# Optimization experiments

Hardware: AMD Instinct MI355X
Metric: run time of the kernel (lower is better)

Reference implementation:

```python
import jax, jax.numpy as jnp
import numpy as np

NEAR = 0.1
FAR = 100.0


def quat_to_rotmat(q):
    q = q / jnp.linalg.norm(q, axis=-1, keepdims=True)
    w, x, y, z = q[..., 0], q[..., 1], q[..., 2], q[..., 3]
    R = jnp.stack([
        1 - 2 * (y * y + z * z), 2 * (x * y - z * w), 2 * (x * z + y * w),
        2 * (x * y + z * w), 1 - 2 * (x * x + z * z), 2 * (y * z - x * w),
        2 * (x * z - y * w), 2 * (y * z + x * w), 1 - 2 * (x * x + y * y)
    ], axis=-1)
    return R.reshape(q.shape[:-1] + (3, 3))


def _render_view(means, scales, rots, opac, sem, E, K3, H, W):
    # means [N,3] ego; E [4,4] ego2cam; K3 [3,3]
    means_cam = means @ E[:3, :3].T + E[:3, 3]  # [N,3]
    x_c, y_c, z = means_cam[:, 0], means_cam[:, 1], means_cam[:, 2]
    z_safe = jnp.maximum(z, 1e-4)
    fx, fy, cx, cy = K3[0, 0], K3[1, 1], K3[0, 2], K3[1, 2]
    u = x_c / z_safe * fx + cx
    v = y_c / z_safe * fy + cy
    # 3D covariance: Sigma = R diag(s)^2 R^T
    R = quat_to_rotmat(rots)              # [N,3,3]
    RS = R * scales[:, None, :]
    Sigma = RS @ jnp.swapaxes(RS, -1, -2)  # [N,3,3]
    Wc = E[:3, :3]
    Sigma_cam = jnp.einsum('ij,njk,lk->nil', Wc, Sigma, Wc)  # [N,3,3]
    # EWA Jacobian J [N,2,3]
    zero = jnp.zeros_like(z)
    J = jnp.stack([
        jnp.stack([fx / z_safe, zero, -fx * x_c / z_safe ** 2], axis=-1),
        jnp.stack([zero, fy / z_safe, -fy * y_c / z_safe ** 2], axis=-1),
    ], axis=-2)
    cov2d = jnp.einsum('nij,njk,nlk->nil', J, Sigma_cam, J)  # [N,2,2]
    a = jnp.maximum(cov2d[:, 0, 0], 0.3)
    c = jnp.maximum(cov2d[:, 1, 1], 0.3)
    bb = cov2d[:, 0, 1]
    det = a * c - bb * bb
    valid = (z > 0.01) & (det > 1e-8)
    det_s = jnp.where(det > 1e-8, det, 1.0)
    ia, ib, ic = c / det_s, -bb / det_s, a / det_s  # inverse 2x2 cov
    # per-pixel Mahalanobis distance, [N,H,W]
    px = jnp.arange(W, dtype=means.dtype)
    py = jnp.arange(H, dtype=means.dtype)
    dx = px[None, None, :] - u[:, None, None]   # [N,1,W]
    dy = py[None, :, None] - v[:, None, None]   # [N,H,1]
    d2 = (ia[:, None, None] * dx * dx + ic[:, None, None] * dy * dy
          + 2.0 * ib[:, None, None] * (dx * dy))
    g = jnp.exp(-0.5 * d2)
    visible = valid & (z > NEAR) & (u >= 0) & (u < W) & (v >= 0) & (v < H)
    alpha = jnp.where(visible[:, None, None],
                      jnp.clip(opac[:, None, None] * g, 0.0, 0.99), 0.0)
    # depth-sorted front-to-back alpha blending
    order = jnp.argsort(z)
    alpha_s = alpha[order]                                     # [N,H,W]
    feats = jnp.concatenate([sem, jnp.clip(z, NEAR, FAR)[:, None]], axis=-1)[order]  # [N,C+1]
    log1m = jnp.log1p(-alpha_s)
    T_excl = jnp.exp(jnp.cumsum(log1m, axis=0) - log1m)        # exclusive transmittance
    wgt = T_excl * alpha_s                                     # [N,H,W]
    rendered = jnp.einsum('nhw,nd->dhw', wgt, feats)           # [C+1,H,W]
    alpha_map = jnp.sum(wgt, axis=0)                           # [H,W]
    C = sem.shape[1]
    return rendered[C:C + 1], rendered[:C], alpha_map[None]


def reference(means, scales, rotations, opacities, semantic_features,
              target_intrinsics, target_cam2ego, H, W):
    ego2cam = jnp.linalg.inv(target_cam2ego)  # [B,M,4,4]
    B, M = target_cam2ego.shape[:2]
    deps, sems, alps = [], [], []
    for b in range(B):
        db, sb, ab = [], [], []
        for m in range(M):
            d, s, a = _render_view(means[b], scales[b], rotations[b],
                                   opacities[b, :, 0], semantic_features[b],
                                   ego2cam[b, m], target_intrinsics[b, m, :3, :3], H, W)
            db.append(d); sb.append(s); ab.append(a)
        deps.append(jnp.stack(db)); sems.append(jnp.stack(sb)); alps.append(jnp.stack(ab))
    depth_map = jnp.stack(deps)     # [B,M,1,H,W]
    semantic_map = jnp.stack(sems)  # [B,M,C,H,W]
    alpha_map = jnp.stack(alps)     # [B,M,1,H,W]
    return depth_map, semantic_map, alpha_map


def setup_inputs() -> dict:
    key = jax.random.key(0)
    ks = jax.random.split(key, 8)
    B, N, C, M, H, W = 1, 2048, 16, 2, 128, 128
    fx = fy = 128.0
    cx = cy = 64.0
    # gaussians inside the frustum: z in [2,40], |x|,|y| < 0.45*z
    z = jax.random.uniform(ks[0], (B, N), minval=2.0, maxval=40.0)
    x = z * jax.random.uniform(ks[1], (B, N), minval=-0.45, maxval=0.45)
    y = z * jax.random.uniform(ks[2], (B, N), minval=-0.45, maxval=0.45)
    means = jnp.stack([x, y, z], axis=-1).astype(jnp.float32)
    scales = jax.random.uniform(ks[3], (B, N, 3), minval=0.05, maxval=0.5).astype(jnp.float32)
    rotations = jax.random.normal(ks[4], (B, N, 4), dtype=jnp.float32)
    opacities = jax.random.uniform(ks[5], (B, N, 1), minval=0.05, maxval=0.95).astype(jnp.float32)
    semantic_features = jax.random.normal(ks[6], (B, N, C), dtype=jnp.float32)
    K = jnp.array([[fx, 0, cx, 0], [0, fy, cy, 0], [0, 0, 1, 0], [0, 0, 0, 1]], dtype=jnp.float32)
    target_intrinsics = jnp.broadcast_to(K, (B, M, 4, 4))
    c2e0 = jnp.eye(4, dtype=jnp.float32)
    c2e1 = c2e0.at[0, 3].set(0.5)
    target_cam2ego = jnp.broadcast_to(jnp.stack([c2e0, c2e1]), (B, M, 4, 4))
    return {"means": means, "scales": scales, "rotations": rotations,
            "opacities": opacities, "semantic_features": semantic_features,
            "target_intrinsics": target_intrinsics, "target_cam2ego": target_cam2ego,
            "H": H, "W": W}
```

## Files before the change

### kernel.cpp

```cpp
#include <hip/hip_runtime.h>
#include <cmath>


#define MAXC   16
#define MAXBM  8
#define NSEG   16
#define RTPB   (NSEG * 64)
#define ROWS1  9
#define ROWS2  10
#define INVIS_KEY 0x7FFFFFFF

__device__ __forceinline__ float rlf(float x, int l) {
    return __int_as_float(__builtin_amdgcn_readlane(__float_as_int(x), l));
}

__device__ void inv4x4_rows3(const float* __restrict__ src, float* __restrict__ Eout) {
    double m[16];
#pragma unroll
    for (int j = 0; j < 16; ++j) m[j] = (double)src[j];
    double inv[16];
    inv[0]  =  m[5]*m[10]*m[15] - m[5]*m[11]*m[14] - m[9]*m[6]*m[15] + m[9]*m[7]*m[14] + m[13]*m[6]*m[11] - m[13]*m[7]*m[10];
    inv[4]  = -m[4]*m[10]*m[15] + m[4]*m[11]*m[14] + m[8]*m[6]*m[15] - m[8]*m[7]*m[14] - m[12]*m[6]*m[11] + m[12]*m[7]*m[10];
    inv[8]  =  m[4]*m[9]*m[15]  - m[4]*m[11]*m[13] - m[8]*m[5]*m[15] + m[8]*m[7]*m[13] + m[12]*m[5]*m[11] - m[12]*m[7]*m[9];
    inv[12] = -m[4]*m[9]*m[14]  + m[4]*m[10]*m[13] + m[8]*m[5]*m[14] - m[8]*m[6]*m[13] - m[12]*m[5]*m[10] + m[12]*m[6]*m[9];
    inv[1]  = -m[1]*m[10]*m[15] + m[1]*m[11]*m[14] + m[9]*m[2]*m[15] - m[9]*m[3]*m[14] - m[13]*m[2]*m[11] + m[13]*m[3]*m[10];
    inv[5]  =  m[0]*m[10]*m[15] - m[0]*m[11]*m[14] - m[8]*m[2]*m[15] + m[8]*m[3]*m[14] + m[12]*m[2]*m[11] - m[12]*m[3]*m[10];
    inv[9]  = -m[0]*m[9]*m[15]  + m[0]*m[11]*m[13] + m[8]*m[1]*m[15] - m[8]*m[3]*m[13] - m[12]*m[1]*m[11] + m[12]*m[3]*m[9];
    inv[13] =  m[0]*m[9]*m[14]  - m[0]*m[10]*m[13] - m[8]*m[1]*m[14] + m[8]*m[2]*m[13] + m[12]*m[1]*m[10] - m[12]*m[2]*m[9];
    inv[2]  =  m[1]*m[6]*m[15]  - m[1]*m[7]*m[14]  - m[5]*m[2]*m[15] + m[5]*m[3]*m[14] + m[13]*m[2]*m[7]  - m[13]*m[3]*m[6];
    inv[6]  = -m[0]*m[6]*m[15]  + m[0]*m[7]*m[14]  + m[4]*m[2]*m[15] - m[4]*m[3]*m[14] - m[12]*m[2]*m[7]  + m[12]*m[3]*m[6];
    inv[10] =  m[0]*m[5]*m[15]  - m[0]*m[7]*m[13]  - m[4]*m[1]*m[15] + m[4]*m[3]*m[13] + m[12]*m[1]*m[7]  - m[12]*m[3]*m[5];
    inv[14] = -m[0]*m[5]*m[14]  + m[0]*m[6]*m[13]  + m[4]*m[1]*m[14] - m[4]*m[2]*m[13] - m[12]*m[1]*m[6]  + m[12]*m[2]*m[5];
    inv[3]  = -m[1]*m[6]*m[11]  + m[1]*m[7]*m[10]  + m[5]*m[2]*m[11] - m[5]*m[3]*m[10] - m[9]*m[2]*m[7]   + m[9]*m[3]*m[6];
    inv[7]  =  m[0]*m[6]*m[11]  - m[0]*m[7]*m[10]  - m[4]*m[2]*m[11] + m[4]*m[3]*m[10] + m[8]*m[2]*m[7]   - m[8]*m[3]*m[6];
    inv[11] = -m[0]*m[5]*m[11]  + m[0]*m[7]*m[9]   + m[4]*m[1]*m[11] - m[4]*m[3]*m[9]  - m[8]*m[1]*m[7]   + m[8]*m[3]*m[5];
    inv[15] =  m[0]*m[5]*m[10]  - m[0]*m[6]*m[9]   - m[4]*m[1]*m[10] + m[4]*m[2]*m[9]  + m[8]*m[1]*m[6]   - m[8]*m[2]*m[5];
    double det = m[0]*inv[0] + m[1]*inv[4] + m[2]*inv[8] + m[3]*inv[12];
    double rdet = 1.0 / det;
#pragma unroll
    for (int r = 0; r < 3; ++r)
#pragma unroll
        for (int c = 0; c < 4; ++c)
            Eout[r * 4 + c] = (float)(inv[r * 4 + c] * rdet);
}

__global__ __launch_bounds__(256) void preprocess_kernel(
    const float* __restrict__ means, const float* __restrict__ scales,
    const float* __restrict__ rots,  const float* __restrict__ intr,
    const float* __restrict__ cam2ego,
    int* __restrict__ ikey, float* __restrict__ uu, float* __restrict__ vv,
    float* __restrict__ cia, float* __restrict__ cib, float* __restrict__ cic,
    float* __restrict__ pr2, int B, int M, int N, int W, int H)
{
    __shared__ float Esh[MAXBM * 12];
    int BM = B * M;
    if (threadIdx.x < (unsigned)BM)
        inv4x4_rows3(cam2ego + (size_t)threadIdx.x * 16, Esh + threadIdx.x * 12);
    __syncthreads();

    int gid = blockIdx.x * 256 + threadIdx.x;
    if (gid >= BM * N) return;
    int bm = gid / N;
    int n  = gid - bm * N;
    int b  = bm / M;
    const float* Ep = Esh + bm * 12;
    const float* mp = means + ((size_t)b * N + n) * 3;
    float mx = mp[0], my = mp[1], mz = mp[2];
    float x_c = Ep[0]*mx + Ep[1]*my + Ep[2]*mz  + Ep[3];
    float y_c = Ep[4]*mx + Ep[5]*my + Ep[6]*mz  + Ep[7];
    float z   = Ep[8]*mx + Ep[9]*my + Ep[10]*mz + Ep[11];
    const float* K = intr + (size_t)bm * 16;
    float fx = K[0], fy = K[5], cx = K[2], cy = K[6];
    float zs = fmaxf(z, 1e-4f);
    float u = x_c / zs * fx + cx;
    float v = y_c / zs * fy + cy;
    const float* qp = rots + ((size_t)b * N + n) * 4;
    float qw = qp[0], qx = qp[1], qy = qp[2], qz = qp[3];
    float qn = sqrtf(qw*qw + qx*qx + qy*qy + qz*qz);
    qw /= qn; qx /= qn; qy /= qn; qz /= qn;
    float R00 = 1.f - 2.f*(qy*qy + qz*qz), R01 = 2.f*(qx*qy - qz*qw), R02 = 2.f*(qx*qz + qy*qw);
    float R10 = 2.f*(qx*qy + qz*qw), R11 = 1.f - 2.f*(qx*qx + qz*qz), R12 = 2.f*(qy*qz - qx*qw);
    float R20 = 2.f*(qx*qz - qy*qw), R21 = 2.f*(qy*qz + qx*qw), R22 = 1.f - 2.f*(qx*qx + qy*qy);
    const float* sp = scales + ((size_t)b * N + n) * 3;
    float s0 = sp[0]*sp[0], s1 = sp[1]*sp[1], s2 = sp[2]*sp[2];
    float S00 = R00*R00*s0 + R01*R01*s1 + R02*R02*s2;
    float S01 = R00*R10*s0 + R01*R11*s1 + R02*R12*s2;
    float S02 = R00*R20*s0 + R01*R21*s1 + R02*R22*s2;
    float S11 = R10*R10*s0 + R11*R11*s1 + R12*R12*s2;
    float S12 = R10*R20*s0 + R11*R21*s1 + R12*R22*s2;
    float S22 = R20*R20*s0 + R21*R21*s1 + R22*R22*s2;
    float W00 = Ep[0], W01 = Ep[1], W02 = Ep[2];
    float W10 = Ep[4], W11 = Ep[5], W12 = Ep[6];
    float W20 = Ep[8], W21 = Ep[9], W22 = Ep[10];
    float A00 = W00*S00 + W01*S01 + W02*S02;
    float A01 = W00*S01 + W01*S11 + W02*S12;
    float A02 = W00*S02 + W01*S12 + W02*S22;
    float A10 = W10*S00 + W11*S01 + W12*S02;
    float A11 = W10*S01 + W11*S11 + W12*S12;
    float A12 = W10*S02 + W11*S12 + W12*S22;
    float A20 = W20*S00 + W21*S01 + W22*S02;
    float A21 = W20*S01 + W21*S11 + W22*S12;
    float A22 = W20*S02 + W21*S12 + W22*S22;
    float Sc00 = A00*W00 + A01*W01 + A02*W02;
    float Sc01 = A00*W10 + A01*W11 + A02*W12;
    float Sc02 = A00*W20 + A01*W21 + A02*W22;
    float Sc11 = A10*W10 + A11*W11 + A12*W12;
    float Sc12 = A10*W20 + A11*W21 + A12*W22;
    float Sc22 = A20*W20 + A21*W21 + A22*W22;
    float j00 = fx / zs,  j02 = -fx * x_c / (zs * zs);
    float j11 = fy / zs,  j12 = -fy * y_c / (zs * zs);
    float c00 = j00*j00*Sc00 + 2.f*j00*j02*Sc02 + j02*j02*Sc22;
    float c01 = j00*(Sc01*j11 + Sc02*j12) + j02*(Sc12*j11 + Sc22*j12);
    float c11 = j11*j11*Sc11 + 2.f*j11*j12*Sc12 + j12*j12*Sc22;
    float a  = fmaxf(c00, 0.3f);
    float cc = fmaxf(c11, 0.3f);
    float bb = c01;
    float det = a * cc - bb * bb;
    bool valid = (z > 0.01f) && (det > 1e-8f);
    float det_s = (det > 1e-8f) ? det : 1.0f;
    float ia = cc / det_s, ib = -bb / det_s, ic = a / det_s;
    uu[gid] = u;  vv[gid] = v;
    cia[gid] = ia;  cib[gid] = ib;  cic[gid] = ic;
    float dmean = 0.5f * (ia + ic);
    float rad   = sqrtf(fmaxf(0.25f*(ia - ic)*(ia - ic) + ib*ib, 0.f));
    float lmin  = fmaxf(dmean - rad, 1e-12f);
    pr2[gid] = 34.0f / lmin;
    bool visible = valid && (z > 0.1f) &&
                   (u >= 0.f) && (u < (float)W) && (v >= 0.f) && (v < (float)H);
    ikey[gid] = visible ? __float_as_int(z) : INVIS_KEY;
}

__global__ __launch_bounds__(64) void rankpack_kernel(
    const int* __restrict__ ikey,
    const float* __restrict__ uu, const float* __restrict__ vv,
    const float* __restrict__ cia, const float* __restrict__ cib,
    const float* __restrict__ cic, const float* __restrict__ pr2,
    const float* __restrict__ opac, const float* __restrict__ sem,
    float* __restrict__ pu, float* __restrict__ pv,
    float* __restrict__ pia, float* __restrict__ pib, float* __restrict__ pic,
    float* __restrict__ pop, float* __restrict__ pdz, float* __restrict__ prr,
    float* __restrict__ psem, int* __restrict__ pcount,
    int B, int M, int N, int C)
{
    int lane  = threadIdx.x & 63;
    int nch64 = (N + 63) >> 6;
    int chunk = blockIdx.x;
    int bm = chunk / nch64;
    int cl = chunk - bm * nch64;
    int i  = (cl << 6) + lane;
    const int* kb = ikey + (size_t)bm * N;
    int ki  = (i < N) ? kb[i] : INVIS_KEY;
    int kip = ki + 1;
    int rank = 0, tot = 0;
    int kj = (lane < N) ? kb[lane] : INVIS_KEY;
    for (int jc = 0; jc < nch64; ++jc) {
        int kcur = kj;
        if (jc + 1 < nch64) {
            int jn = ((jc + 1) << 6) + lane;
            kj = (jn < N) ? kb[jn] : INVIS_KEY;
        }
        tot += (int)__popcll(__ballot(kcur != INVIS_KEY));
        if (jc < cl) {
#pragma unroll
            for (int gg = 0; gg < 64; ++gg)
                rank += (__builtin_amdgcn_readlane(kcur, gg) < kip);
        } else if (jc > cl) {
#pragma unroll
            for (int gg = 0; gg < 64; ++gg)
                rank += (__builtin_amdgcn_readlane(kcur, gg) < ki);
        } else {
#pragma unroll
            for (int gg = 0; gg < 64; ++gg) {
                int kk = (gg < lane) ? kip : ki;
                rank += (__builtin_amdgcn_readlane(kcur, gg) < kk);
            }
        }
    }
    if (cl == 0 && lane == 0) pcount[bm] = tot;
    if (i < N && ki != INVIS_KEY) {
        int b = bm / M;
        size_t src = (size_t)bm * N + i;
        size_t dst = (size_t)bm * N + rank;
        pu[dst]  = uu[src];   pv[dst]  = vv[src];
        pia[dst] = cia[src];  pib[dst] = cib[src];  pic[dst] = cic[src];
        pop[dst] = opac[(size_t)b * N + i];
        float z  = __int_as_float(ki);
        pdz[dst] = fminf(fmaxf(z, 0.1f), 100.0f);
        prr[dst] = pr2[src];
        const float* spc = sem + ((size_t)b * N + i) * C;
        float* dpc = psem + dst * C;
        int c4 = C & ~3;
        for (int q = 0; q < c4; q += 4)
            *(float4*)(dpc + q) = *(const float4*)(spc + q);
        for (int q = c4; q < C; ++q) dpc[q] = spc[q];
    }
}

__global__ __launch_bounds__(RTPB) void raster_kernel(
    const float* __restrict__ pu, const float* __restrict__ pv,
    const float* __restrict__ pia, const float* __restrict__ pib,
    const float* __restrict__ pic, const float* __restrict__ pop,
    const float* __restrict__ pdz, const float* __restrict__ prr,
    const float* __restrict__ psem, const int* __restrict__ pcount,
    float* __restrict__ out,
    int BM, int N, int C, int H, int W, int ntx, int nty)
{
    __shared__ float comb[NSEG * ROWS2 * 64];
    int wave = threadIdx.x >> 6;
    int lane = threadIdx.x & 63;
    int tile = blockIdx.x;
    int tpv = ntx * nty;
    int bm  = tile / tpv;
    int rem = tile - bm * tpv;
    int tyi = rem / ntx;
    int txi = rem - tyi * ntx;
    int lx = lane & 7, ly = lane >> 3;
    float fxp = (float)(txi * 8 + lx), fyp = (float)(tyi * 8 + ly);
    float x0 = (float)(txi * 8),     y0 = (float)(tyi * 8);
    float x1 = (float)(txi * 8 + 7), y1 = (float)(tyi * 8 + 7);

    int cnt = pcount[bm];
    int seg = (cnt + NSEG - 1) / NSEG;
    int gs = wave * seg;
    int ge = min(gs + seg, cnt);

    float T = 1.0f, accA = 0.f, accD = 0.f;
    float accS[MAXC];
#pragma unroll
    for (int q = 0; q < MAXC; ++q) accS[q] = 0.f;

    for (int base = gs; base < ge; base += 64) {
        if (!__any(T >= 1e-6f)) break;
        int g = base + lane;
        bool inr = g < ge;
        size_t src = (size_t)bm * N + g;
        float gu = 1e30f, gv = 1e30f, gia = 0.f, gib = 0.f, gic = 0.f,
              gop = 0.f, gdz = 0.f, gr2 = -1.f;
        if (inr) {
            gu  = pu[src];  gv  = pv[src];
            gia = pia[src]; gib = pib[src]; gic = pic[src];
            gop = pop[src]; gdz = pdz[src]; gr2 = prr[src];
        }
        float cxm = fminf(fmaxf(gu, x0), x1);
        float cym = fminf(fmaxf(gv, y0), y1);
        float ddx = gu - cxm, ddy = gv - cym;
        float dist2 = ddx*ddx + ddy*ddy;
        unsigned long long mask = __ballot(inr && (dist2 <= gr2));
        float sf[MAXC];
        if ((mask >> lane) & 1ull) {
            const float4* spc = (const float4*)(psem + src * MAXC);
#pragma unroll
            for (int q = 0; q < MAXC / 4; ++q) {
                float4 f = spc[q];
                sf[q*4+0] = f.x; sf[q*4+1] = f.y; sf[q*4+2] = f.z; sf[q*4+3] = f.w;
            }
        }
        while (mask) {
            int gg = __ffsll(mask) - 1;
            mask &= mask - 1;
            float u  = rlf(gu, gg),  v  = rlf(gv, gg);
            float ia = rlf(gia, gg), ib = rlf(gib, gg), ic = rlf(gic, gg);
            float dx = fxp - u, dy = fyp - v;
            float d2 = ia*dx*dx + ic*dy*dy + 2.0f*ib*(dx*dy);
            float gvl = __expf(-0.5f * d2);
            float alpha = fminf(rlf(gop, gg) * gvl, 0.99f);
            float w = T * alpha;
            T -= w;
            accD += w * rlf(gdz, gg);
            accA += w;
#pragma unroll
            for (int ch = 0; ch < MAXC; ++ch) accS[ch] += w * rlf(sf[ch], gg);
        }
    }

    int px = lane;
    int pxx = txi * 8 + (px & 7);
    int pyy = tyi * 8 + (px >> 3);
    bool inb = (pxx < W) && (pyy < H);
    size_t HW  = (size_t)H * W;
    size_t pix = (size_t)pyy * W + pxx;
    size_t BMHW = (size_t)BM * HW;

    float* my = comb + (wave * ROWS1) * 64 + lane;
    my[0 * 64] = T;
    my[1 * 64] = accD;
    my[2 * 64] = accA;
#pragma unroll
    for (int k = 0; k < 6; ++k) my[(3 + k) * 64] = accS[k];
    __syncthreads();

    float pre[NSEG];
    pre[0] = 1.f;
#pragma unroll
    for (int w = 1; w < NSEG; ++w)
        pre[w] = pre[w-1] * comb[((w-1) * ROWS1) * 64 + px];

    if (wave < 8) {
        int row, outc;
        if (wave == 0)      { row = 1;        outc = 0; }
        else if (wave <= 6) { row = 2 + wave; outc = wave; }
        else                { row = 2;        outc = C + 1; }
        float val = 0.f;
#pragma unroll
        for (int w = 0; w < NSEG; ++w)
            val += pre[w] * comb[(w * ROWS1 + row) * 64 + px];
        if (inb) {
            float* dst;
            if (outc == 0)      dst = out + (size_t)bm * HW + pix;
            else if (outc <= C) dst = out + BMHW + (size_t)bm * C * HW + (size_t)(outc-1) * HW + pix;
            else                dst = out + BMHW + BMHW * C + (size_t)bm * HW + pix;
            *dst = val;
        }
    }
    __syncthreads();

    float* my2 = comb + (wave * ROWS2) * 64 + lane;
#pragma unroll
    for (int k = 0; k < 10; ++k) my2[k * 64] = accS[6 + k];
    __syncthreads();

    if (wave < 10) {
        int k = wave;
        float val = 0.f;
#pragma unroll
        for (int w = 0; w < NSEG; ++w)
            val += pre[w] * comb[(w * ROWS2 + k) * 64 + px];
        if (inb) {
            int outc = 7 + k;
            float* dst = out + BMHW + (size_t)bm * C * HW + (size_t)(outc-1) * HW + pix;
            *dst = val;
        }
    }
}

extern "C" void kernel_launch(void* const* d_in, const int* in_sizes, int n_in,
                              void* d_out, int out_size, void* d_ws, size_t ws_size,
                              hipStream_t stream) {
    const float* means  = (const float*)d_in[0];
    const float* scales = (const float*)d_in[1];
    const float* rots   = (const float*)d_in[2];
    const float* opac   = (const float*)d_in[3];
    const float* sem    = (const float*)d_in[4];
    const float* intr   = (const float*)d_in[5];
    const float* c2e    = (const float*)d_in[6];
    float* out = (float*)d_out;

    int B  = 1;
    int BM = in_sizes[6] / 16;
    int M  = BM / B;
    int N  = in_sizes[0] / (3 * B);
    int C  = in_sizes[4] / (B * N);
    long HWl = (long)out_size / ((long)BM * (C + 2));
    int H = (int)(sqrt((double)HWl) + 0.5);
    int W = (int)(HWl / H);
    int ntx = (W + 7) / 8, nty = (H + 7) / 8;
    int ntiles = ntx * nty * BM;
    int nch64  = (N + 63) >> 6;

    float* ws = (float*)d_ws;
    size_t off = 0;
    size_t BMN  = (size_t)BM * N;
    int*   ikey = (int*)(ws + off); off += BMN;
    float* uu   = ws + off; off += BMN;
    float* vv   = ws + off; off += BMN;
    float* cia  = ws + off; off += BMN;
    float* cib  = ws + off; off += BMN;
    float* cic  = ws + off; off += BMN;
    float* pr2  = ws + off; off += BMN;
    float* pu   = ws + off; off += BMN;
    float* pv   = ws + off; off += BMN;
    float* pia  = ws + off; off += BMN;
    float* pib  = ws + off; off += BMN;
    float* pic  = ws + off; off += BMN;
    float* pop  = ws + off; off += BMN;
    float* pdz  = ws + off; off += BMN;
    float* prr  = ws + off; off += BMN;
    float* psem = ws + off; off += BMN * C;
    int* pcount = (int*)(ws + off); off += BM;

    int tot = BM * N;
    preprocess_kernel<<<(tot + 255) / 256, 256, 0, stream>>>(
        means, scales, rots, intr, c2e,
        ikey, uu, vv, cia, cib, cic, pr2, B, M, N, W, H);

    rankpack_kernel<<<BM * nch64, 64, 0, stream>>>(
        ikey, uu, vv, cia, cib, cic, pr2, opac, sem,
        pu, pv, pia, pib, pic, pop, pdz, prr, psem, pcount, B, M, N, C);

    raster_kernel<<<ntiles, RTPB, 0, stream>>>(
        pu, pv, pia, pib, pic, pop, pdz, prr, psem, pcount, out,
        BM, N, C, H, W, ntx, nty);
}
```

Measured before the change: 131.7 us.

## Cull gaussians per tile with exact ellipse-rectangle test instead of bounding circle

Replaces the conservative circular radius test (based on the smallest eigenvalue of the inverse covariance) with an axis-aligned ellipse bounding box plus an exact minimum Mahalanobis distance over the tile rectangle, computed from per-edge conditional minimizers. Preprocess and rankpack now produce four per-gaussian values (x/y extents and two conditional-slope coefficients) instead of one radius. The goal is fewer gaussians entering the serial per-lane blend loop. The cost is more memory traffic and more ALU work per candidate in the cull step. It also switches the semantic accumulators to float2 pairs, which probably makes no difference.

```diff
diff --git a/kernel.cpp b/kernel.cpp
--- a/kernel.cpp
+++ b/kernel.cpp
@@ -50,7 +50,9 @@
     const float* __restrict__ cam2ego,
     int* __restrict__ ikey, float* __restrict__ uu, float* __restrict__ vv,
     float* __restrict__ cia, float* __restrict__ cib, float* __restrict__ cic,
-    float* __restrict__ pr2, int B, int M, int N, int W, int H)
+    float* __restrict__ cex, float* __restrict__ cey,
+    float* __restrict__ crbc, float* __restrict__ crba,
+    int B, int M, int N, int W, int H)
 {
     __shared__ float Esh[MAXBM * 12];
     int BM = B * M;
@@ -121,10 +123,10 @@
     float ia = cc / det_s, ib = -bb / det_s, ic = a / det_s;
     uu[gid] = u;  vv[gid] = v;
     cia[gid] = ia;  cib[gid] = ib;  cic[gid] = ic;
-    float dmean = 0.5f * (ia + ic);
-    float rad   = sqrtf(fmaxf(0.25f*(ia - ic)*(ia - ic) + ib*ib, 0.f));
-    float lmin  = fmaxf(dmean - rad, 1e-12f);
-    pr2[gid] = 34.0f / lmin;
+    cex[gid] = sqrtf(34.0f * a);
+    cey[gid] = sqrtf(34.0f * cc);
+    crbc[gid] = -bb / a;
+    crba[gid] = -bb / cc;
     bool visible = valid && (z > 0.1f) &&
                    (u >= 0.f) && (u < (float)W) && (v >= 0.f) && (v < (float)H);
     ikey[gid] = visible ? __float_as_int(z) : INVIS_KEY;
@@ -134,11 +136,15 @@
     const int* __restrict__ ikey,
     const float* __restrict__ uu, const float* __restrict__ vv,
     const float* __restrict__ cia, const float* __restrict__ cib,
-    const float* __restrict__ cic, const float* __restrict__ pr2,
+    const float* __restrict__ cic, const float* __restrict__ cex,
+    const float* __restrict__ cey, const float* __restrict__ crbc,
+    const float* __restrict__ crba,
     const float* __restrict__ opac, const float* __restrict__ sem,
     float* __restrict__ pu, float* __restrict__ pv,
     float* __restrict__ pia, float* __restrict__ pib, float* __restrict__ pic,
-    float* __restrict__ pop, float* __restrict__ pdz, float* __restrict__ prr,
+    float* __restrict__ pop, float* __restrict__ pdz,
+    float* __restrict__ pex, float* __restrict__ pey,
+    float* __restrict__ prbc, float* __restrict__ prba,
     float* __restrict__ psem, int* __restrict__ pcount,
     int B, int M, int N, int C)
 {
@@ -186,7 +192,8 @@
         pop[dst] = opac[(size_t)b * N + i];
         float z  = __int_as_float(ki);
         pdz[dst] = fminf(fmaxf(z, 0.1f), 100.0f);
-        prr[dst] = pr2[src];
+        pex[dst]  = cex[src];  pey[dst]  = cey[src];
+        prbc[dst] = crbc[src]; prba[dst] = crba[src];
         const float* spc = sem + ((size_t)b * N + i) * C;
         float* dpc = psem + dst * C;
         int c4 = C & ~3;
@@ -200,7 +207,9 @@
     const float* __restrict__ pu, const float* __restrict__ pv,
     const float* __restrict__ pia, const float* __restrict__ pib,
     const float* __restrict__ pic, const float* __restrict__ pop,
-    const float* __restrict__ pdz, const float* __restrict__ prr,
+    const float* __restrict__ pdz,
+    const float* __restrict__ pex, const float* __restrict__ pey,
+    const float* __restrict__ prbc, const float* __restrict__ prba,
     const float* __restrict__ psem, const int* __restrict__ pcount,
     float* __restrict__ out,
     int BM, int N, int C, int H, int W, int ntx, int nty)
@@ -225,9 +234,9 @@
     int ge = min(gs + seg, cnt);
 
     float T = 1.0f, accA = 0.f, accD = 0.f;
-    float accS[MAXC];
-#pragma unroll
-    for (int q = 0; q < MAXC; ++q) accS[q] = 0.f;
+    float2 accS2[MAXC / 2];
+#pragma unroll
+    for (int q = 0; q < MAXC / 2; ++q) accS2[q] = make_float2(0.f, 0.f);
 
     for (int base = gs; base < ge; base += 64) {
         if (!__any(T >= 1e-6f)) break;
@@ -235,17 +244,30 @@
         bool inr = g < ge;
         size_t src = (size_t)bm * N + g;
         float gu = 1e30f, gv = 1e30f, gia = 0.f, gib = 0.f, gic = 0.f,
-              gop = 0.f, gdz = 0.f, gr2 = -1.f;
+              gop = 0.f, gdz = 0.f, gex = -1.f, gey = -1.f,
+              grbc = 0.f, grba = 0.f;
         if (inr) {
             gu  = pu[src];  gv  = pv[src];
             gia = pia[src]; gib = pib[src]; gic = pic[src];
-            gop = pop[src]; gdz = pdz[src]; gr2 = prr[src];
-        }
-        float cxm = fminf(fmaxf(gu, x0), x1);
-        float cym = fminf(fmaxf(gv, y0), y1);
-        float ddx = gu - cxm, ddy = gv - cym;
-        float dist2 = ddx*ddx + ddy*ddy;
-        unsigned long long mask = __ballot(inr && (dist2 <= gr2));
+            gop = pop[src]; gdz = pdz[src];
+            gex = pex[src]; gey = pey[src];
+            grbc = prbc[src]; grba = prba[src];
+        }
+        float dx0 = x0 - gu, dx1 = x1 - gu;
+        float dy0 = y0 - gv, dy1 = y1 - gv;
+        bool aabb = (dx0 <= gex) && (-dx1 <= gex) && (dy0 <= gey) && (-dy1 <= gey);
+        bool inside = (dx0 <= 0.f) && (dx1 >= 0.f) && (dy0 <= 0.f) && (dy1 >= 0.f);
+        float t, q0, q1, q2, q3;
+        t  = fminf(fmaxf(grbc * dx0, dy0), dy1);
+        q0 = gia * dx0 * dx0 + t * (gic * t + 2.f * gib * dx0);
+        t  = fminf(fmaxf(grbc * dx1, dy0), dy1);
+        q1 = gia * dx1 * dx1 + t * (gic * t + 2.f * gib * dx1);
+        t  = fminf(fmaxf(grba * dy0, dx0), dx1);
+        q2 = gic * dy0 * dy0 + t * (gia * t + 2.f * gib * dy0);
+        t  = fminf(fmaxf(grba * dy1, dx0), dx1);
+        q3 = gic * dy1 * dy1 + t * (gia * t + 2.f * gib * dy1);
+        float mind2 = inside ? 0.f : fminf(fminf(q0, q1), fminf(q2, q3));
+        unsigned long long mask = __ballot(aabb && (mind2 <= 34.0f));
         float sf[MAXC];
         if ((mask >> lane) & 1ull) {
             const float4* spc = (const float4*)(psem + src * MAXC);
@@ -269,8 +291,17 @@
             accD += w * rlf(gdz, gg);
             accA += w;
 #pragma unroll
-            for (int ch = 0; ch < MAXC; ++ch) accS[ch] += w * rlf(sf[ch], gg);
-        }
+            for (int q = 0; q < MAXC / 2; ++q) {
+                float2 f = make_float2(rlf(sf[2*q], gg), rlf(sf[2*q+1], gg));
+                accS2[q].x += w * f.x;
+                accS2[q].y += w * f.y;
+            }
+        }
+    }
+    float accS[MAXC];
+#pragma unroll
+    for (int q = 0; q < MAXC / 2; ++q) {
+        accS[2*q] = accS2[q].x; accS[2*q+1] = accS2[q].y;
     }
 
     int px = lane;
@@ -366,7 +397,10 @@
     float* cia  = ws + off; off += BMN;
     float* cib  = ws + off; off += BMN;
     float* cic  = ws + off; off += BMN;
-    float* pr2  = ws + off; off += BMN;
+    float* cex  = ws + off; off += BMN;
+    float* cey  = ws + off; off += BMN;
+    float* crbc = ws + off; off += BMN;
+    float* crba = ws + off; off += BMN;
     float* pu   = ws + off; off += BMN;
     float* pv   = ws + off; off += BMN;
     float* pia  = ws + off; off += BMN;
@@ -374,20 +408,24 @@
     float* pic  = ws + off; off += BMN;
     float* pop  = ws + off; off += BMN;
     float* pdz  = ws + off; off += BMN;
-    float* prr  = ws + off; off += BMN;
+    float* pex  = ws + off; off += BMN;
+    float* pey  = ws + off; off += BMN;
+    float* prbc = ws + off; off += BMN;
+    float* prba = ws + off; off += BMN;
     float* psem = ws + off; off += BMN * C;
     int* pcount = (int*)(ws + off); off += BM;
 
     int tot = BM * N;
     preprocess_kernel<<<(tot + 255) / 256, 256, 0, stream>>>(
         means, scales, rots, intr, c2e,
-        ikey, uu, vv, cia, cib, cic, pr2, B, M, N, W, H);
+        ikey, uu, vv, cia, cib, cic, cex, cey, crbc, crba, B, M, N, W, H);
 
     rankpack_kernel<<<BM * nch64, 64, 0, stream>>>(
-        ikey, uu, vv, cia, cib, cic, pr2, opac, sem,
-        pu, pv, pia, pib, pic, pop, pdz, prr, psem, pcount, B, M, N, C);
+        ikey, uu, vv, cia, cib, cic, cex, cey, crbc, crba, opac, sem,
+        pu, pv, pia, pib, pic, pop, pdz, pex, pey, prbc, prba,
+        psem, pcount, B, M, N, C);
 
     raster_kernel<<<ntiles, RTPB, 0, stream>>>(
-        pu, pv, pia, pib, pic, pop, pdz, prr, psem, pcount, out,
-        BM, N, C, H, W, ntx, nty);
-}
+        pu, pv, pia, pib, pic, pop, pdz, pex, pey, prbc, prba,
+        psem, pcount, out, BM, N, C, H, W, ntx, nty);
+}
```

Result: no change. 133.1 us (+1.1%).

## Split raster depth range across two blocks, tighten culling, pack splat attributes

Applied to the files above, without the earlier changes.

Each tile's sorted splat list is now split into two halves handled by separate 512-thread blocks. Each block writes partial transmittance and accumulations, and a new combine kernel composites the two halves. Per-splat culling changes from an isotropic radius test to an axis-aligned bounding box plus an exact minimum-Mahalanobis-distance test over the tile rectangle. Splat attributes are also packed into three float4 arrays for wider loads. The aim is more blocks in flight, fewer false-positive splats and fewer scattered loads, at the cost of an extra launch and partial-result traffic through global memory.

```diff
diff --git a/kernel.cpp b/kernel.cpp
--- a/kernel.cpp
+++ b/kernel.cpp
@@ -4,10 +4,12 @@
 
 #define MAXC   16
 #define MAXBM  8
-#define NSEG   16
-#define RTPB   (NSEG * 64)
+#define NSEGL  8
+#define NHALF  2
+#define RTPB   (NSEGL * 64)
 #define ROWS1  9
 #define ROWS2  10
+#define PROWS  19
 #define INVIS_KEY 0x7FFFFFFF
 
 __device__ __forceinline__ float rlf(float x, int l) {
@@ -50,7 +52,9 @@
     const float* __restrict__ cam2ego,
     int* __restrict__ ikey, float* __restrict__ uu, float* __restrict__ vv,
     float* __restrict__ cia, float* __restrict__ cib, float* __restrict__ cic,
-    float* __restrict__ pr2, int B, int M, int N, int W, int H)
+    float* __restrict__ cex, float* __restrict__ cey,
+    float* __restrict__ crbc, float* __restrict__ crba,
+    int B, int M, int N, int W, int H)
 {
     __shared__ float Esh[MAXBM * 12];
     int BM = B * M;
@@ -121,10 +125,10 @@
     float ia = cc / det_s, ib = -bb / det_s, ic = a / det_s;
     uu[gid] = u;  vv[gid] = v;
     cia[gid] = ia;  cib[gid] = ib;  cic[gid] = ic;
-    float dmean = 0.5f * (ia + ic);
-    float rad   = sqrtf(fmaxf(0.25f*(ia - ic)*(ia - ic) + ib*ib, 0.f));
-    float lmin  = fmaxf(dmean - rad, 1e-12f);
-    pr2[gid] = 34.0f / lmin;
+    cex[gid] = sqrtf(34.0f * a);
+    cey[gid] = sqrtf(34.0f * cc);
+    crbc[gid] = -bb / a;
+    crba[gid] = -bb / cc;
     bool visible = valid && (z > 0.1f) &&
                    (u >= 0.f) && (u < (float)W) && (v >= 0.f) && (v < (float)H);
     ikey[gid] = visible ? __float_as_int(z) : INVIS_KEY;
@@ -134,11 +138,12 @@
     const int* __restrict__ ikey,
     const float* __restrict__ uu, const float* __restrict__ vv,
     const float* __restrict__ cia, const float* __restrict__ cib,
-    const float* __restrict__ cic, const float* __restrict__ pr2,
+    const float* __restrict__ cic, const float* __restrict__ cex,
+    const float* __restrict__ cey, const float* __restrict__ crbc,
+    const float* __restrict__ crba,
     const float* __restrict__ opac, const float* __restrict__ sem,
-    float* __restrict__ pu, float* __restrict__ pv,
-    float* __restrict__ pia, float* __restrict__ pib, float* __restrict__ pic,
-    float* __restrict__ pop, float* __restrict__ pdz, float* __restrict__ prr,
+    float4* __restrict__ pk0, float4* __restrict__ pk1,
+    float4* __restrict__ pk2,
     float* __restrict__ psem, int* __restrict__ pcount,
     int B, int M, int N, int C)
 {
@@ -181,12 +186,12 @@
         int b = bm / M;
         size_t src = (size_t)bm * N + i;
         size_t dst = (size_t)bm * N + rank;
-        pu[dst]  = uu[src];   pv[dst]  = vv[src];
-        pia[dst] = cia[src];  pib[dst] = cib[src];  pic[dst] = cic[src];
-        pop[dst] = opac[(size_t)b * N + i];
-        float z  = __int_as_float(ki);
-        pdz[dst] = fminf(fmaxf(z, 0.1f), 100.0f);
-        prr[dst] = pr2[src];
+        float z = __int_as_float(ki);
+        pk0[dst] = make_float4(uu[src], vv[src], cex[src], cey[src]);
+        pk1[dst] = make_float4(cia[src], cib[src], cic[src],
+                               opac[(size_t)b * N + i]);
+        pk2[dst] = make_float4(fminf(fmaxf(z, 0.1f), 100.0f),
+                               crbc[src], crba[src], 0.f);
         const float* spc = sem + ((size_t)b * N + i) * C;
         float* dpc = psem + dst * C;
         int c4 = C & ~3;
@@ -196,19 +201,19 @@
     }
 }
 
-__global__ __launch_bounds__(RTPB) void raster_kernel(
-    const float* __restrict__ pu, const float* __restrict__ pv,
-    const float* __restrict__ pia, const float* __restrict__ pib,
-    const float* __restrict__ pic, const float* __restrict__ pop,
-    const float* __restrict__ pdz, const float* __restrict__ prr,
+__global__ __launch_bounds__(RTPB) void raster_partial_kernel(
+    const float4* __restrict__ pk0, const float4* __restrict__ pk1,
+    const float4* __restrict__ pk2,
     const float* __restrict__ psem, const int* __restrict__ pcount,
-    float* __restrict__ out,
+    float* __restrict__ part,
     int BM, int N, int C, int H, int W, int ntx, int nty)
 {
-    __shared__ float comb[NSEG * ROWS2 * 64];
+    __shared__ float comb[NSEGL * ROWS2 * 64];
     int wave = threadIdx.x >> 6;
     int lane = threadIdx.x & 63;
-    int tile = blockIdx.x;
+    int bh   = blockIdx.x;
+    int tile = bh >> 1;
+    int half = bh & 1;
     int tpv = ntx * nty;
     int bm  = tile / tpv;
     int rem = tile - bm * tpv;
@@ -220,8 +225,9 @@
     float x1 = (float)(txi * 8 + 7), y1 = (float)(tyi * 8 + 7);
 
     int cnt = pcount[bm];
-    int seg = (cnt + NSEG - 1) / NSEG;
-    int gs = wave * seg;
+    int seg = (cnt + NSEGL * NHALF - 1) / (NSEGL * NHALF);
+    int wg  = half * NSEGL + wave;
+    int gs = wg * seg;
     int ge = min(gs + seg, cnt);
 
     float T = 1.0f, accA = 0.f, accD = 0.f;
@@ -233,19 +239,27 @@
         if (!__any(T >= 1e-6f)) break;
         int g = base + lane;
         bool inr = g < ge;
-        size_t src = (size_t)bm * N + g;
-        float gu = 1e30f, gv = 1e30f, gia = 0.f, gib = 0.f, gic = 0.f,
-              gop = 0.f, gdz = 0.f, gr2 = -1.f;
-        if (inr) {
-            gu  = pu[src];  gv  = pv[src];
-            gia = pia[src]; gib = pib[src]; gic = pic[src];
-            gop = pop[src]; gdz = pdz[src]; gr2 = prr[src];
-        }
-        float cxm = fminf(fmaxf(gu, x0), x1);
-        float cym = fminf(fmaxf(gv, y0), y1);
-        float ddx = gu - cxm, ddy = gv - cym;
-        float dist2 = ddx*ddx + ddy*ddy;
-        unsigned long long mask = __ballot(inr && (dist2 <= gr2));
+        int gc = inr ? g : (ge - 1);
+        size_t src = (size_t)bm * N + gc;
+        float4 P0 = pk0[src];
+        float4 P1 = pk1[src];
+        float4 P2 = pk2[src];
+        float dx0 = x0 - P0.x, dx1 = x1 - P0.x;
+        float dy0 = y0 - P0.y, dy1 = y1 - P0.y;
+        bool aabb = (dx0 <= P0.z) && (-dx1 <= P0.z) &&
+                    (dy0 <= P0.w) && (-dy1 <= P0.w);
+        bool inside = (dx0 <= 0.f) && (dx1 >= 0.f) && (dy0 <= 0.f) && (dy1 >= 0.f);
+        float t, q0, q1, q2, q3;
+        t  = fminf(fmaxf(P2.y * dx0, dy0), dy1);
+        q0 = P1.x * dx0 * dx0 + t * (P1.z * t + 2.f * P1.y * dx0);
+        t  = fminf(fmaxf(P2.y * dx1, dy0), dy1);
+        q1 = P1.x * dx1 * dx1 + t * (P1.z * t + 2.f * P1.y * dx1);
+        t  = fminf(fmaxf(P2.z * dy0, dx0), dx1);
+        q2 = P1.z * dy0 * dy0 + t * (P1.x * t + 2.f * P1.y * dy0);
+        t  = fminf(fmaxf(P2.z * dy1, dx0), dx1);
+        q3 = P1.z * dy1 * dy1 + t * (P1.x * t + 2.f * P1.y * dy1);
+        float mind2 = inside ? 0.f : fminf(fminf(q0, q1), fminf(q2, q3));
+        unsigned long long mask = __ballot(inr && aabb && (mind2 <= 34.0f));
         float sf[MAXC];
         if ((mask >> lane) & 1ull) {
             const float4* spc = (const float4*)(psem + src * MAXC);
@@ -258,29 +272,22 @@
         while (mask) {
             int gg = __ffsll(mask) - 1;
             mask &= mask - 1;
-            float u  = rlf(gu, gg),  v  = rlf(gv, gg);
-            float ia = rlf(gia, gg), ib = rlf(gib, gg), ic = rlf(gic, gg);
+            float u  = rlf(P0.x, gg), v  = rlf(P0.y, gg);
+            float ia = rlf(P1.x, gg), ib = rlf(P1.y, gg), ic = rlf(P1.z, gg);
             float dx = fxp - u, dy = fyp - v;
             float d2 = ia*dx*dx + ic*dy*dy + 2.0f*ib*(dx*dy);
             float gvl = __expf(-0.5f * d2);
-            float alpha = fminf(rlf(gop, gg) * gvl, 0.99f);
+            float alpha = fminf(rlf(P1.w, gg) * gvl, 0.99f);
             float w = T * alpha;
             T -= w;
-            accD += w * rlf(gdz, gg);
+            accD += w * rlf(P2.x, gg);
             accA += w;
 #pragma unroll
             for (int ch = 0; ch < MAXC; ++ch) accS[ch] += w * rlf(sf[ch], gg);
         }
     }
 
-    int px = lane;
-    int pxx = txi * 8 + (px & 7);
-    int pyy = tyi * 8 + (px >> 3);
-    bool inb = (pxx < W) && (pyy < H);
-    size_t HW  = (size_t)H * W;
-    size_t pix = (size_t)pyy * W + pxx;
-    size_t BMHW = (size_t)BM * HW;
-
+    float* pout = part + (size_t)bh * (PROWS * 64);
     float* my = comb + (wave * ROWS1) * 64 + lane;
     my[0 * 64] = T;
     my[1 * 64] = accD;
@@ -289,28 +296,24 @@
     for (int k = 0; k < 6; ++k) my[(3 + k) * 64] = accS[k];
     __syncthreads();
 
-    float pre[NSEG];
+    int px = lane;
+    float pre[NSEGL];
     pre[0] = 1.f;
 #pragma unroll
-    for (int w = 1; w < NSEG; ++w)
+    for (int w = 1; w < NSEGL; ++w)
         pre[w] = pre[w-1] * comb[((w-1) * ROWS1) * 64 + px];
 
-    if (wave < 8) {
-        int row, outc;
-        if (wave == 0)      { row = 1;        outc = 0; }
-        else if (wave <= 6) { row = 2 + wave; outc = wave; }
-        else                { row = 2;        outc = C + 1; }
-        float val = 0.f;
-#pragma unroll
-        for (int w = 0; w < NSEG; ++w)
-            val += pre[w] * comb[(w * ROWS1 + row) * 64 + px];
-        if (inb) {
-            float* dst;
-            if (outc == 0)      dst = out + (size_t)bm * HW + pix;
-            else if (outc <= C) dst = out + BMHW + (size_t)bm * C * HW + (size_t)(outc-1) * HW + pix;
-            else                dst = out + BMHW + BMHW * C + (size_t)bm * HW + pix;
-            *dst = val;
+    for (int o = wave; o < 9; o += NSEGL) {
+        float val;
+        if (o == 0) {
+            val = pre[NSEGL-1] * comb[((NSEGL-1) * ROWS1) * 64 + px];
+        } else {
+            val = 0.f;
+#pragma unroll
+            for (int w = 0; w < NSEGL; ++w)
+                val += pre[w] * comb[(w * ROWS1 + o) * 64 + px];
         }
+        pout[o * 64 + px] = val;
     }
     __syncthreads();
 
@@ -319,18 +322,40 @@
     for (int k = 0; k < 10; ++k) my2[k * 64] = accS[6 + k];
     __syncthreads();
 
-    if (wave < 10) {
-        int k = wave;
+    for (int o = wave; o < 10; o += NSEGL) {
         float val = 0.f;
 #pragma unroll
-        for (int w = 0; w < NSEG; ++w)
-            val += pre[w] * comb[(w * ROWS2 + k) * 64 + px];
-        if (inb) {
-            int outc = 7 + k;
-            float* dst = out + BMHW + (size_t)bm * C * HW + (size_t)(outc-1) * HW + pix;
-            *dst = val;
-        }
+        for (int w = 0; w < NSEGL; ++w)
+            val += pre[w] * comb[(w * ROWS2 + o) * 64 + px];
+        pout[(9 + o) * 64 + px] = val;
     }
+}
+
+__global__ __launch_bounds__(64) void combine_kernel(
+    const float* __restrict__ part, float* __restrict__ out,
+    int BM, int C, int H, int W, int ntx, int nty)
+{
+    int tile = blockIdx.x;
+    int px   = threadIdx.x;
+    int tpv = ntx * nty;
+    int bm  = tile / tpv;
+    int rem = tile - bm * tpv;
+    int tyi = rem / ntx;
+    int txi = rem - tyi * ntx;
+    int pxx = txi * 8 + (px & 7);
+    int pyy = tyi * 8 + (px >> 3);
+    if (pxx >= W || pyy >= H) return;
+    size_t HW  = (size_t)H * W;
+    size_t pix = (size_t)pyy * W + pxx;
+    size_t BMHW = (size_t)BM * HW;
+    const float* a = part + (size_t)(tile * 2 + 0) * (PROWS * 64);
+    const float* b = part + (size_t)(tile * 2 + 1) * (PROWS * 64);
+    float T0 = a[0 * 64 + px];
+    out[(size_t)bm * HW + pix] = a[1*64+px] + T0 * b[1*64+px];
+    out[BMHW + BMHW * C + (size_t)bm * HW + pix] = a[2*64+px] + T0 * b[2*64+px];
+    float* semo = out + BMHW + (size_t)bm * C * HW + pix;
+    for (int k = 0; k < C && k < MAXC; ++k)
+        semo[(size_t)k * HW] = a[(3+k)*64+px] + T0 * b[(3+k)*64+px];
 }
 
 extern "C" void kernel_launch(void* const* d_in, const int* in_sizes, int n_in,
@@ -366,28 +391,30 @@
     float* cia  = ws + off; off += BMN;
     float* cib  = ws + off; off += BMN;
     float* cic  = ws + off; off += BMN;
-    float* pr2  = ws + off; off += BMN;
-    float* pu   = ws + off; off += BMN;
-    float* pv   = ws + off; off += BMN;
-    float* pia  = ws + off; off += BMN;
-    float* pib  = ws + off; off += BMN;
-    float* pic  = ws + off; off += BMN;
-    float* pop  = ws + off; off += BMN;
-    float* pdz  = ws + off; off += BMN;
-    float* prr  = ws + off; off += BMN;
+    float* cex  = ws + off; off += BMN;
+    float* cey  = ws + off; off += BMN;
+    float* crbc = ws + off; off += BMN;
+    float* crba = ws + off; off += BMN;
+    off = (off + 3) & ~(size_t)3;
+    float4* pk0 = (float4*)(ws + off); off += BMN * 4;
+    float4* pk1 = (float4*)(ws + off); off += BMN * 4;
+    float4* pk2 = (float4*)(ws + off); off += BMN * 4;
     float* psem = ws + off; off += BMN * C;
-    int* pcount = (int*)(ws + off); off += BM;
+    int* pcount = (int*)(ws + off); off += BM + 3;
+    float* part = ws + off; off += (size_t)ntiles * 2 * PROWS * 64;
 
     int tot = BM * N;
     preprocess_kernel<<<(tot + 255) / 256, 256, 0, stream>>>(
         means, scales, rots, intr, c2e,
-        ikey, uu, vv, cia, cib, cic, pr2, B, M, N, W, H);
+        ikey, uu, vv, cia, cib, cic, cex, cey, crbc, crba, B, M, N, W, H);
 
     rankpack_kernel<<<BM * nch64, 64, 0, stream>>>(
-        ikey, uu, vv, cia, cib, cic, pr2, opac, sem,
-        pu, pv, pia, pib, pic, pop, pdz, prr, psem, pcount, B, M, N, C);
-
-    raster_kernel<<<ntiles, RTPB, 0, stream>>>(
-        pu, pv, pia, pib, pic, pop, pdz, prr, psem, pcount, out,
-        BM, N, C, H, W, ntx, nty);
-}
+        ikey, uu, vv, cia, cib, cic, cex, cey, crbc, crba, opac, sem,
+        pk0, pk1, pk2, psem, pcount, B, M, N, C);
+
+    raster_partial_kernel<<<ntiles * 2, RTPB, 0, stream>>>(
+        pk0, pk1, pk2, psem, pcount, part, BM, N, C, H, W, ntx, nty);
+
+    combine_kernel<<<ntiles, 64, 0, stream>>>(
+        part, out, BM, C, H, W, ntx, nty);
+}
```

Measured after the change: 145.6 us. 10.6% more time.
